# Kernel tuning notes

Measured on AMD Instinct MI355X. Metric: run time of the kernel, lower is better.

## Reference

```python
import jax, jax.numpy as jnp
import numpy as np


def _pose_encoding(N, d, dtype):
    # Faithful to original formula: angle = idx / (1000*(2*(k/d)) + 0.01)
    idx = jnp.arange(N, dtype=jnp.float32)[:, None]            # [N,1]
    if d % 2 == 0:
        sin_d = cos_d = d // 2
    else:
        sin_d = (d - 1) // 2 + 1
        cos_d = (d - 1) // 2
    k_sin = jnp.arange(sin_d, dtype=jnp.float32)[None, :]      # [1,sin_d]
    k_cos = jnp.arange(cos_d, dtype=jnp.float32)[None, :]      # [1,cos_d]
    denom_sin = 1000.0 * (2.0 * (k_sin / d)) + 0.01
    denom_cos = 1000.0 * (2.0 * (k_cos / d)) + 0.01
    sin_ape = jnp.sin(idx / denom_sin)                          # [N,sin_d]
    cos_ape = jnp.cos(idx / denom_cos)                          # [N,cos_d]
    pe = jnp.zeros((N, d), dtype=jnp.float32)
    pe = pe.at[:, 0::2].set(sin_ape)
    pe = pe.at[:, 1::2].set(cos_ape)
    return pe.astype(dtype)


def setup_inputs() -> dict:
    key = jax.random.key(0)
    B, S, N, d = 8, 16, 1024, 256
    x = jax.random.normal(key, (B, S, N, d), dtype=jnp.float32)
    return {"x": x}


def reference(x) -> jnp.ndarray:
    B, S, N, d = x.shape
    pe = _pose_encoding(N, d, x.dtype)                          # [N,d], broadcast over B,S
    return x + pe
```

## Files before the change

kernel.cpp:

```cpp
#include <hip/hip_runtime.h>


#define N4_TOTAL (8 * 16 * 1024 * 256 / 4)

__global__ __launch_bounds__(256) void pose_add_kernel(
    const float4* __restrict__ x, float4* __restrict__ out) {
    int i = blockIdx.x * blockDim.x + threadIdx.x;
    if (i >= N4_TOTAL) return;

    int c4 = i & 63;
    int n  = (i >> 6) & 1023;
    float fn = (float)n;

    int   k0     = c4 << 1;
    float denom0 = 7.8125f * (float)k0 + 0.01f;
    float denom1 = 7.8125f * (float)(k0 + 1) + 0.01f;
    float a0 = fn / denom0;
    float a1 = fn / denom1;

    float4 v = x[i];
    float4 r;
    r.x = v.x + __sinf(a0);
    r.y = v.y + __cosf(a0);
    r.z = v.z + __sinf(a1);
    r.w = v.w + __cosf(a1);
    out[i] = r;
}

extern "C" void kernel_launch(void* const* d_in, const int* in_sizes, int n_in,
                              void* d_out, int out_size, void* d_ws, size_t ws_size,
                              hipStream_t stream) {
    const float4* x   = (const float4*)d_in[0];
    float4*       out = (float4*)d_out;
    int blocks = (N4_TOTAL + 255) / 256;
    pose_add_kernel<<<blocks, 256, 0, stream>>>(x, out);
}
```

Baseline: 217.4 us.

## Compute positional encoding once per position and reuse across batch rows

The grid is restructured so each block owns one position n and 64 of the 128 batch*seq slices. The block computes the 256-element encoding row once into shared memory, then every thread adds it to 16 strided rows. This removes the per-element divisions and sin/cos work but adds a barrier and strided access across batch slices, and it launches far fewer threads. The kernel is memory-bound, so any gain from dropping transcendental math is likely small.

```diff
diff --git a/kernel.cpp b/kernel.cpp
--- a/kernel.cpp
+++ b/kernel.cpp
@@ -1,30 +1,52 @@
 #include <hip/hip_runtime.h>
 
 
-#define N4_TOTAL (8 * 16 * 1024 * 256 / 4)
+#define NPOS 1024
+#define D4   64
+#define BS   128
+#define BS_PER_BLOCK 64
 
 __global__ __launch_bounds__(256) void pose_add_kernel(
     const float4* __restrict__ x, float4* __restrict__ out) {
-    int i = blockIdx.x * blockDim.x + threadIdx.x;
-    if (i >= N4_TOTAL) return;
+    __shared__ float4 pe[D4];
 
-    int c4 = i & 63;
-    int n  = (i >> 6) & 1023;
-    float fn = (float)n;
+    const int n = blockIdx.x;
+    const int t = threadIdx.x;
 
-    int   k0     = c4 << 1;
-    float denom0 = 7.8125f * (float)k0 + 0.01f;
-    float denom1 = 7.8125f * (float)(k0 + 1) + 0.01f;
-    float a0 = fn / denom0;
-    float a1 = fn / denom1;
+    if (t < D4) {
+        float fn = (float)n;
+        int   k0 = t << 1;
+        float d0 = 7.8125f * (float)k0 + 0.01f;
+        float d1 = 7.8125f * (float)(k0 + 1) + 0.01f;
+        float a0 = fn / d0;
+        float a1 = fn / d1;
+        float4 p;
+        p.x = __sinf(a0);
+        p.y = __cosf(a0);
+        p.z = __sinf(a1);
+        p.w = __cosf(a1);
+        pe[t] = p;
+    }
+    __syncthreads();
 
-    float4 v = x[i];
-    float4 r;
-    r.x = v.x + __sinf(a0);
-    r.y = v.y + __cosf(a0);
-    r.z = v.z + __sinf(a1);
-    r.w = v.w + __cosf(a1);
-    out[i] = r;
+    const int c4 = t & 63;
+    const int r0 = t >> 6;
+    const float4 p = pe[c4];
+
+    const int    bs_base = blockIdx.y * BS_PER_BLOCK;
+    const size_t row_off = (size_t)n * D4 + c4;
+
+#pragma unroll 4
+    for (int j = r0; j < BS_PER_BLOCK; j += 4) {
+        size_t idx = (size_t)(bs_base + j) * (NPOS * D4) + row_off;
+        float4 v = x[idx];
+        float4 r;
+        r.x = v.x + p.x;
+        r.y = v.y + p.y;
+        r.z = v.z + p.z;
+        r.w = v.w + p.w;
+        out[idx] = r;
+    }
 }
 
 extern "C" void kernel_launch(void* const* d_in, const int* in_sizes, int n_in,
@@ -32,6 +54,6 @@
                               hipStream_t stream) {
     const float4* x   = (const float4*)d_in[0];
     float4*       out = (float4*)d_out;
-    int blocks = (N4_TOTAL + 255) / 256;
-    pose_add_kernel<<<blocks, 256, 0, stream>>>(x, out);
+    dim3 grid(NPOS, BS / BS_PER_BLOCK);
+    pose_add_kernel<<<grid, 256, 0, stream>>>(x, out);
 }
```

Measured after the change: 228.8 us. 5.2% more time.
